# Performance work log

Hardware: AMD Instinct MI355X
Metric: run time of the kernel (lower is better)

The kernel has to match this reference:

```python
import jax, jax.numpy as jnp
import numpy as np

DIM = 768


def setup_inputs() -> dict:
    key = jax.random.key(0)
    k1, k2, k3, k4, k5 = jax.random.split(key, 5)
    lines = jax.random.normal(k1, (32, 512, DIM), dtype=jnp.float32)
    videos = jax.random.normal(k2, (32, 128, DIM), dtype=jnp.float32)
    video_mask = jax.random.randint(k3, (32, 128), 0, 2, dtype=jnp.int32)
    # nn.Linear(dim, dim, bias=False) weights, applied as x @ W.T
    w_q = jax.random.normal(k4, (DIM, DIM), dtype=jnp.float32) * (DIM ** -0.5)
    w_k = jax.random.normal(k5, (DIM, DIM), dtype=jnp.float32) * (DIM ** -0.5)
    return {"lines": lines, "videos": videos, "video_mask": video_mask, "w_q": w_q, "w_k": w_k}


def reference(lines, videos, video_mask, w_q, w_k):
    scale = DIM ** -0.5
    q = jnp.einsum('bld,ed->ble', lines, w_q)   # (B, L, D)
    k = jnp.einsum('bvd,ed->bve', videos, w_k)  # (B, V, D)
    scores = jnp.einsum('bld,bvd->blv', q, k) * scale
    pad = (video_mask == 0)[:, None, :]          # (B, 1, V)
    scores = jnp.where(pad, jnp.float32(-1e9), scores)
    weights = jax.nn.softmax(scores, axis=-1)    # (B, L, V)
    return jnp.einsum('blv,bvd->bld', weights, videos)
```

## Files before the change

### kernel.cpp

```cpp
#include <hip/hip_runtime.h>

#define DIM 768
#define NB  32
#define LQ  512
#define NV  128

typedef unsigned short u16;
typedef unsigned int   u32;
typedef __bf16 bf16x8 __attribute__((ext_vector_type(8)));
typedef float  f32x4  __attribute__((ext_vector_type(4)));
typedef u16    u16x8  __attribute__((ext_vector_type(8)));
typedef u16    u16x4  __attribute__((ext_vector_type(4)));

typedef __attribute__((address_space(1))) const void gvoid;
typedef __attribute__((address_space(3))) void       svoid;

__device__ __forceinline__ u16 f2bf(float f) {
    u32 u = __float_as_uint(f);
    return (u16)((u + 0x7FFFu + ((u >> 16) & 1u)) >> 16);
}

__device__ __forceinline__ bf16x8 ld_frag(const u16* p) {
    return __builtin_bit_cast(bf16x8, *(const u16x8*)p);
}

__device__ __forceinline__ void gld16(const void* g, void* l) {
    __builtin_amdgcn_global_load_lds((gvoid*)g, (svoid*)l, 16, 0, 0);
}

#define W2_BLK 36
#define NL_BLK 6144

__global__ __launch_bounds__(256) void prep_kernel(const float* __restrict__ lines,
                                                   const float* __restrict__ w_q,
                                                   const float* __restrict__ w_k,
                                                   const float* __restrict__ videos,
                                                   u16* __restrict__ lbf,
                                                   u16* __restrict__ w2b,
                                                   u16* __restrict__ vt2,
                                                   u16* __restrict__ vbf) {
    __shared__ union {
        u16 T[64][136];
        struct { u16 q[128][72]; u16 k[128][72]; } w2s;
    } uL;
    const int bx = blockIdx.x;
    const int t  = threadIdx.x;

    if (bx < W2_BLK) {
        const int m0 = (bx / 6) * 128;
        const int n0 = (bx % 6) * 128;
        const int w    = t >> 6;
        const int lane = t & 63;
        const int quad = lane >> 4;
        const int ln   = lane & 15;
        const int wr   = (w >> 1) * 64;
        const int wc   = (w & 1) * 64;
        f32x4 acc[4][4] = {};
        for (int ks = 0; ks < 12; ++ks) {
            __syncthreads();
            const int e0 = ks * 64;
#pragma unroll
            for (int p = 0; p < 8; ++p) {
                int f  = t + p * 256;
                int r  = f >> 5;
                int c4 = f & 31;
                float4 xq = *(const float4*)(w_q + (size_t)(e0 + r) * DIM + m0 + c4 * 4);
                float4 xk = *(const float4*)(w_k + (size_t)(e0 + r) * DIM + n0 + c4 * 4);
                uL.w2s.q[c4 * 4 + 0][r] = f2bf(xq.x);
                uL.w2s.q[c4 * 4 + 1][r] = f2bf(xq.y);
                uL.w2s.q[c4 * 4 + 2][r] = f2bf(xq.z);
                uL.w2s.q[c4 * 4 + 3][r] = f2bf(xq.w);
                uL.w2s.k[c4 * 4 + 0][r] = f2bf(xk.x);
                uL.w2s.k[c4 * 4 + 1][r] = f2bf(xk.y);
                uL.w2s.k[c4 * 4 + 2][r] = f2bf(xk.z);
                uL.w2s.k[c4 * 4 + 3][r] = f2bf(xk.w);
            }
            __syncthreads();
#pragma unroll
            for (int kk = 0; kk < 2; ++kk) {
                bf16x8 af[4], bfr[4];
#pragma unroll
                for (int i = 0; i < 4; ++i) af[i]  = ld_frag(&uL.w2s.q[wr + i * 16 + ln][kk * 32 + quad * 8]);
#pragma unroll
                for (int j = 0; j < 4; ++j) bfr[j] = ld_frag(&uL.w2s.k[wc + j * 16 + ln][kk * 32 + quad * 8]);
#pragma unroll
                for (int i = 0; i < 4; ++i)
#pragma unroll
                    for (int j = 0; j < 4; ++j)
                        acc[i][j] = __builtin_amdgcn_mfma_f32_16x16x32_bf16(af[i], bfr[j], acc[i][j], 0, 0, 0);
            }
        }
#pragma unroll
        for (int i = 0; i < 4; ++i)
#pragma unroll
            for (int j = 0; j < 4; ++j)
#pragma unroll
                for (int r = 0; r < 4; ++r)
                    w2b[(size_t)(m0 + wr + i * 16 + quad * 4 + r) * DIM + n0 + wc + j * 16 + ln] =
                        f2bf(acc[i][j][r]);
        return;
    }

    if (bx < W2_BLK + NL_BLK) {
        size_t i = (size_t)(bx - W2_BLK) * 256 + t;
        float4 a = ((const float4*)lines)[i * 2];
        float4 b = ((const float4*)lines)[i * 2 + 1];
        u16x8 o = { f2bf(a.x), f2bf(a.y), f2bf(a.z), f2bf(a.w),
                    f2bf(b.x), f2bf(b.y), f2bf(b.z), f2bf(b.w) };
        ((u16x8*)lbf)[i] = o;
        return;
    }

    const int v  = bx - (W2_BLK + NL_BLK);
    const int b  = v / 12;
    const int d0 = (v % 12) * 64;
    const float* src = videos + (size_t)b * NV * DIM;
#pragma unroll
    for (int p = 0; p < 8; ++p) {
        int f  = t + p * 256;
        int vv = f >> 4;
        int c4 = f & 15;
        float4 x = *(const float4*)(src + (size_t)vv * DIM + d0 + c4 * 4);
        u16x4 o = { f2bf(x.x), f2bf(x.y), f2bf(x.z), f2bf(x.w) };
        uL.T[c4 * 4 + 0][vv] = o[0];
        uL.T[c4 * 4 + 1][vv] = o[1];
        uL.T[c4 * 4 + 2][vv] = o[2];
        uL.T[c4 * 4 + 3][vv] = o[3];
        *(u16x4*)(vbf + ((size_t)b * NV + vv) * DIM + d0 + c4 * 4) = o;
    }
    __syncthreads();
#pragma unroll
    for (int p = 0; p < 4; ++p) {
        int f  = t + p * 256;
        int dl = f >> 4;
        int v8 = f & 15;
        int d  = d0 + dl;
        int it = d >> 7, wv = (d >> 4) & 7, lnn = d & 15;
        int ks = v8 >> 2, qd = v8 & 3;
        int lane = qd * 16 + lnn;
        size_t off = ((((size_t)b * 6 + it) * 8 + wv) * 4 + ks) * 512 + lane * 8;
        *(u16x8*)(vt2 + off) = *(const u16x8*)&uL.T[dl][v8 * 8];
    }
}

__global__ __launch_bounds__(512) void g_kernel(const u16* __restrict__ A,
                                                const u16* __restrict__ W,
                                                u16* __restrict__ C) {
    __shared__ u16 sA[128][64];
    __shared__ u16 sB[128][64];
    const int t    = threadIdx.x;
    const int w    = t >> 6;
    const int lane = t & 63;
    const int quad = lane >> 4;
    const int ln   = lane & 15;

    int m0, n0;
    {
        int i = blockIdx.x;
        int xcd = i & 7, s = i >> 3;
        m0 = ((s / 6) * 8 + xcd) * 128;
        n0 = (s % 6) * 128;
    }

    const int wr = (w >> 2) * 64;
    const int wc = (w & 3) * 32;
    const int srow   = lane >> 3;
    const int schunk = (lane & 7) ^ srow;

    f32x4 acc[4][2] = {};
#pragma unroll
    for (int ks = 0; ks < 12; ++ks) {
        __syncthreads();
#pragma unroll
        for (int p = 0; p < 2; ++p) {
            int rb = w * 16 + p * 8;
            gld16(A + (size_t)(m0 + rb + srow) * DIM + ks * 64 + schunk * 8, &sA[rb][0]);
            gld16(W + (size_t)(n0 + rb + srow) * DIM + ks * 64 + schunk * 8, &sB[rb][0]);
        }
        __syncthreads();
#pragma unroll
        for (int kk = 0; kk < 2; ++kk) {
            bf16x8 af[4], bfr[2];
#pragma unroll
            for (int i = 0; i < 4; ++i)
                af[i]  = ld_frag(&sA[wr + i * 16 + ln][((kk * 4 + quad) ^ (ln & 7)) * 8]);
#pragma unroll
            for (int j = 0; j < 2; ++j)
                bfr[j] = ld_frag(&sB[wc + j * 16 + ln][((kk * 4 + quad) ^ (ln & 7)) * 8]);
#pragma unroll
            for (int i = 0; i < 4; ++i)
#pragma unroll
                for (int j = 0; j < 2; ++j)
                    acc[i][j] = __builtin_amdgcn_mfma_f32_16x16x32_bf16(af[i], bfr[j], acc[i][j], 0, 0, 0);
        }
    }
#pragma unroll
    for (int i = 0; i < 4; ++i)
#pragma unroll
        for (int j = 0; j < 2; ++j)
#pragma unroll
            for (int r = 0; r < 4; ++r)
                C[(size_t)(m0 + wr + i * 16 + quad * 4 + r) * DIM + n0 + wc + j * 16 + ln] =
                    f2bf(acc[i][j][r]);
}

__global__ __launch_bounds__(512) void attn_kernel(const u16* __restrict__ Q,
                                                   const u16* __restrict__ K,
                                                   const u16* __restrict__ Vt2,
                                                   const int* __restrict__ mask,
                                                   float* __restrict__ out) {
    int b, l0;
    {
        int i = blockIdx.x;
        int xcd = i & 7, s = i >> 3;
        b  = (s >> 3) * 8 + xcd;
        l0 = (s & 7) * 64;
    }
    const int t    = threadIdx.x;
    const int w    = t >> 6;
    const int lane = t & 63;
    const int quad = lane >> 4;
    const int ln   = lane & 15;

    __shared__ union {
        struct { u16 q[64][64]; u16 k[128][64]; } st;
        float s[64][132];
    } uA;
    __shared__ union {
        struct { u16 q[64][64]; u16 k[128][64]; } st;
        u16 p[64][136];
    } uB;
    __shared__ float sBias[128];

    const u16* Qb = Q + ((size_t)b * LQ + l0) * DIM;
    const u16* Kb = K + (size_t)b * NV * DIM;
    if (t < NV) sBias[t] = mask[b * NV + t] ? 0.0f : -1e9f;

    const int srow   = lane >> 3;
    const int schunk = (lane & 7) ^ srow;

    auto stage = [&](int ks, int sel) {
        u16 (*q)[64] = sel ? uB.st.q : uA.st.q;
        u16 (*k)[64] = sel ? uB.st.k : uA.st.k;
        gld16(Qb + (size_t)(w * 8 + srow) * DIM + ks * 64 + schunk * 8, &q[w * 8][0]);
        gld16(Kb + (size_t)(w * 16 + srow) * DIM + ks * 64 + schunk * 8, &k[w * 16][0]);
        gld16(Kb + (size_t)(w * 16 + 8 + srow) * DIM + ks * 64 + schunk * 8, &k[w * 16 + 8][0]);
    };

    f32x4 accS[4] = {};
    stage(0, 0);
#pragma unroll
    for (int ks = 0; ks < 12; ++ks) {
        __syncthreads();
        if (ks < 11) stage(ks + 1, (ks + 1) & 1);
        u16 (*q)[64] = (ks & 1) ? uB.st.q : uA.st.q;
        u16 (*k)[64] = (ks & 1) ? uB.st.k : uA.st.k;
#pragma unroll
        for (int kk = 0; kk < 2; ++kk) {
            bf16x8 bfr = ld_frag(&k[w * 16 + ln][((kk * 4 + quad) ^ (ln & 7)) * 8]);
#pragma unroll
            for (int i = 0; i < 4; ++i) {
                bf16x8 af = ld_frag(&q[i * 16 + ln][((kk * 4 + quad) ^ (ln & 7)) * 8]);
                accS[i] = __builtin_amdgcn_mfma_f32_16x16x32_bf16(af, bfr, accS[i], 0, 0, 0);
            }
        }
    }
    __syncthreads();
    const float scale = 0.03608439182435161f;
#pragma unroll
    for (int i = 0; i < 4; ++i)
#pragma unroll
        for (int r = 0; r < 4; ++r)
            uA.s[i * 16 + quad * 4 + r][w * 16 + ln] = accS[i][r] * scale;
    __syncthreads();

    {
        const int row = t >> 3, seg = t & 7;
        float vals[16];
        float mx = -3.0e38f;
#pragma unroll
        for (int c = 0; c < 4; ++c) {
            float4 x  = *(const float4*)&uA.s[row][seg * 16 + c * 4];
            float4 bz = *(const float4*)&sBias[seg * 16 + c * 4];
            float a0 = x.x + bz.x, a1 = x.y + bz.y, a2 = x.z + bz.z, a3 = x.w + bz.w;
            vals[c * 4 + 0] = a0; vals[c * 4 + 1] = a1;
            vals[c * 4 + 2] = a2; vals[c * 4 + 3] = a3;
            mx = fmaxf(mx, fmaxf(fmaxf(a0, a1), fmaxf(a2, a3)));
        }
        mx = fmaxf(mx, __shfl_xor(mx, 1));
        mx = fmaxf(mx, __shfl_xor(mx, 2));
        mx = fmaxf(mx, __shfl_xor(mx, 4));
        float sum = 0.0f;
#pragma unroll
        for (int c = 0; c < 16; ++c) { float e = __expf(vals[c] - mx); vals[c] = e; sum += e; }
        sum += __shfl_xor(sum, 1);
        sum += __shfl_xor(sum, 2);
        sum += __shfl_xor(sum, 4);
        const float inv = 1.0f / sum;
        __syncthreads();
#pragma unroll
        for (int h = 0; h < 2; ++h) {
            u16x8 pk;
#pragma unroll
            for (int e = 0; e < 8; ++e) pk[e] = f2bf(vals[h * 8 + e] * inv);
            *(u16x8*)&uB.p[row][seg * 16 + h * 8] = pk;
        }
    }
    __syncthreads();

    bf16x8 paf[4][4];
#pragma unroll
    for (int i = 0; i < 4; ++i)
#pragma unroll
        for (int ks = 0; ks < 4; ++ks)
            paf[i][ks] = ld_frag(&uB.p[i * 16 + ln][ks * 32 + quad * 8]);

    const u16* V2 = Vt2 + (size_t)b * 6 * 8 * 4 * 512;
    float*     Ob = out + ((size_t)b * LQ + l0) * DIM;
    for (int it = 0; it < 6; ++it) {
        f32x4 accO[4] = {};
#pragma unroll
        for (int ks = 0; ks < 4; ++ks) {
            bf16x8 bv = ld_frag(V2 + (((size_t)(it * 8 + w)) * 4 + ks) * 512 + lane * 8);
#pragma unroll
            for (int i = 0; i < 4; ++i)
                accO[i] = __builtin_amdgcn_mfma_f32_16x16x32_bf16(paf[i][ks], bv, accO[i], 0, 0, 0);
        }
#pragma unroll
        for (int i = 0; i < 4; ++i)
#pragma unroll
            for (int r = 0; r < 4; ++r)
                Ob[(size_t)(i * 16 + quad * 4 + r) * DIM + it * 128 + w * 16 + ln] = accO[i][r];
    }
}

extern "C" void kernel_launch(void* const* d_in, const int* in_sizes, int n_in,
                              void* d_out, int out_size, void* d_ws, size_t ws_size,
                              hipStream_t stream) {
    const float* lines  = (const float*)d_in[0];
    const float* videos = (const float*)d_in[1];
    const int*   mask   = (const int*)d_in[2];
    const float* w_q    = (const float*)d_in[3];
    const float* w_k    = (const float*)d_in[4];
    float*       out    = (float*)d_out;

    u16* gw  = (u16*)d_ws;
    u16* vt2 = gw  + (size_t)NB * NV * DIM;
    u16* lbf = vt2 + (size_t)NB * DIM * NV;
    u16* vbf = lbf + (size_t)NB * LQ * DIM;
    u16* w2b = vbf + (size_t)NB * NV * DIM;

    prep_kernel<<<W2_BLK + NL_BLK + 384, 256, 0, stream>>>(
        lines, w_q, w_k, videos, lbf, w2b, vt2, vbf);
    g_kernel   <<<192, 512, 0, stream>>>(vbf, w2b, gw);
    attn_kernel<<<256, 512, 0, stream>>>(lbf, gw, vt2, mask, out);
}
```

Measured before the change: 192.6 us.

## Split W_q^T W_k product over K with atomic fp32 accumulation and swizzled LDS

The W2 = Wq^T·Wk tile blocks are split four ways along the reduction dimension, so 144 blocks run instead of 36, and the partial sums are combined with float atomicAdd into an fp32 buffer that is zeroed by a memset first. The LDS tiles in that GEMM get an XOR swizzle to cut bank conflicts on transposed stores and fragment loads. g_kernel now reads the fp32 W2 and converts it to bf16 into a padded, swizzled LDS tile, in place of the async global-to-LDS copy of bf16 data. This is meant to shorten the tail of the prep kernel, where a few long-running W2 blocks finish late. In exchange it adds a memset launch, atomic traffic, and heavier per-block loads and conversion in g_kernel.

```diff
diff --git a/kernel.cpp b/kernel.cpp
--- a/kernel.cpp
+++ b/kernel.cpp
@@ -28,7 +28,8 @@
     __builtin_amdgcn_global_load_lds((gvoid*)g, (svoid*)l, 16, 0, 0);
 }
 
-#define W2_BLK 36
+#define W2S    4
+#define W2_BLK (36 * W2S)
 #define NL_BLK 6144
 
 __global__ __launch_bounds__(256) void prep_kernel(const float* __restrict__ lines,
@@ -36,7 +37,7 @@
                                                    const float* __restrict__ w_k,
                                                    const float* __restrict__ videos,
                                                    u16* __restrict__ lbf,
-                                                   u16* __restrict__ w2b,
+                                                   float* __restrict__ w2f,
                                                    u16* __restrict__ vt2,
                                                    u16* __restrict__ vbf) {
     __shared__ union {
@@ -47,8 +48,9 @@
     const int t  = threadIdx.x;
 
     if (bx < W2_BLK) {
-        const int m0 = (bx / 6) * 128;
-        const int n0 = (bx % 6) * 128;
+        const int tile = bx / W2S, kc = bx % W2S;
+        const int m0 = (tile / 6) * 128;
+        const int n0 = (tile % 6) * 128;
         const int w    = t >> 6;
         const int lane = t & 63;
         const int quad = lane >> 4;
@@ -56,7 +58,7 @@
         const int wr   = (w >> 1) * 64;
         const int wc   = (w & 1) * 64;
         f32x4 acc[4][4] = {};
-        for (int ks = 0; ks < 12; ++ks) {
+        for (int ks = kc * 3; ks < kc * 3 + 3; ++ks) {
             __syncthreads();
             const int e0 = ks * 64;
 #pragma unroll
@@ -66,23 +68,30 @@
                 int c4 = f & 31;
                 float4 xq = *(const float4*)(w_q + (size_t)(e0 + r) * DIM + m0 + c4 * 4);
                 float4 xk = *(const float4*)(w_k + (size_t)(e0 + r) * DIM + n0 + c4 * 4);
-                uL.w2s.q[c4 * 4 + 0][r] = f2bf(xq.x);
-                uL.w2s.q[c4 * 4 + 1][r] = f2bf(xq.y);
-                uL.w2s.q[c4 * 4 + 2][r] = f2bf(xq.z);
-                uL.w2s.q[c4 * 4 + 3][r] = f2bf(xq.w);
-                uL.w2s.k[c4 * 4 + 0][r] = f2bf(xk.x);
-                uL.w2s.k[c4 * 4 + 1][r] = f2bf(xk.y);
-                uL.w2s.k[c4 * 4 + 2][r] = f2bf(xk.z);
-                uL.w2s.k[c4 * 4 + 3][r] = f2bf(xk.w);
+                int swz = ((r >> 3) ^ ((c4 >> 1) & 7)) * 8 + (r & 7);
+                uL.w2s.q[c4 * 4 + 0][swz] = f2bf(xq.x);
+                uL.w2s.q[c4 * 4 + 1][swz] = f2bf(xq.y);
+                uL.w2s.q[c4 * 4 + 2][swz] = f2bf(xq.z);
+                uL.w2s.q[c4 * 4 + 3][swz] = f2bf(xq.w);
+                uL.w2s.k[c4 * 4 + 0][swz] = f2bf(xk.x);
+                uL.w2s.k[c4 * 4 + 1][swz] = f2bf(xk.y);
+                uL.w2s.k[c4 * 4 + 2][swz] = f2bf(xk.z);
+                uL.w2s.k[c4 * 4 + 3][swz] = f2bf(xk.w);
             }
             __syncthreads();
 #pragma unroll
             for (int kk = 0; kk < 2; ++kk) {
                 bf16x8 af[4], bfr[4];
 #pragma unroll
-                for (int i = 0; i < 4; ++i) af[i]  = ld_frag(&uL.w2s.q[wr + i * 16 + ln][kk * 32 + quad * 8]);
-#pragma unroll
-                for (int j = 0; j < 4; ++j) bfr[j] = ld_frag(&uL.w2s.k[wc + j * 16 + ln][kk * 32 + quad * 8]);
+                for (int i = 0; i < 4; ++i) {
+                    int row = wr + i * 16 + ln;
+                    af[i]  = ld_frag(&uL.w2s.q[row][((kk * 4 + quad) ^ ((row >> 3) & 7)) * 8]);
+                }
+#pragma unroll
+                for (int j = 0; j < 4; ++j) {
+                    int row = wc + j * 16 + ln;
+                    bfr[j] = ld_frag(&uL.w2s.k[row][((kk * 4 + quad) ^ ((row >> 3) & 7)) * 8]);
+                }
 #pragma unroll
                 for (int i = 0; i < 4; ++i)
 #pragma unroll
@@ -96,8 +105,8 @@
             for (int j = 0; j < 4; ++j)
 #pragma unroll
                 for (int r = 0; r < 4; ++r)
-                    w2b[(size_t)(m0 + wr + i * 16 + quad * 4 + r) * DIM + n0 + wc + j * 16 + ln] =
-                        f2bf(acc[i][j][r]);
+                    atomicAdd(&w2f[(size_t)(m0 + wr + i * 16 + quad * 4 + r) * DIM +
+                                   n0 + wc + j * 16 + ln], acc[i][j][r]);
         return;
     }
 
@@ -144,10 +153,10 @@
 }
 
 __global__ __launch_bounds__(512) void g_kernel(const u16* __restrict__ A,
-                                                const u16* __restrict__ W,
+                                                const float* __restrict__ Wf,
                                                 u16* __restrict__ C) {
     __shared__ u16 sA[128][64];
-    __shared__ u16 sB[128][64];
+    __shared__ u16 sB[128][72];
     const int t    = threadIdx.x;
     const int w    = t >> 6;
     const int lane = t & 63;
@@ -175,7 +184,15 @@
         for (int p = 0; p < 2; ++p) {
             int rb = w * 16 + p * 8;
             gld16(A + (size_t)(m0 + rb + srow) * DIM + ks * 64 + schunk * 8, &sA[rb][0]);
-            gld16(W + (size_t)(n0 + rb + srow) * DIM + ks * 64 + schunk * 8, &sB[rb][0]);
+        }
+#pragma unroll
+        for (int p = 0; p < 4; ++p) {
+            int idx = t + p * 512;
+            int row = idx >> 4, c4 = idx & 15;
+            float4 x = *(const float4*)(Wf + (size_t)(n0 + row) * DIM + ks * 64 + c4 * 4);
+            u16x4 o = { f2bf(x.x), f2bf(x.y), f2bf(x.z), f2bf(x.w) };
+            int swz = ((c4 >> 1) ^ (row & 7)) * 8 + (c4 & 1) * 4;
+            *(u16x4*)&sB[row][swz] = o;
         }
         __syncthreads();
 #pragma unroll
@@ -344,14 +361,15 @@
     const float* w_k    = (const float*)d_in[4];
     float*       out    = (float*)d_out;
 
-    u16* gw  = (u16*)d_ws;
-    u16* vt2 = gw  + (size_t)NB * NV * DIM;
-    u16* lbf = vt2 + (size_t)NB * DIM * NV;
-    u16* vbf = lbf + (size_t)NB * LQ * DIM;
-    u16* w2b = vbf + (size_t)NB * NV * DIM;
-
+    u16*   gw  = (u16*)d_ws;
+    u16*   vt2 = gw  + (size_t)NB * NV * DIM;
+    u16*   lbf = vt2 + (size_t)NB * DIM * NV;
+    u16*   vbf = lbf + (size_t)NB * LQ * DIM;
+    float* w2f = (float*)(vbf + (size_t)NB * NV * DIM);
+
+    hipMemsetAsync(w2f, 0, (size_t)DIM * DIM * sizeof(float), stream);
     prep_kernel<<<W2_BLK + NL_BLK + 384, 256, 0, stream>>>(
-        lines, w_q, w_k, videos, lbf, w2b, vt2, vbf);
-    g_kernel   <<<192, 512, 0, stream>>>(vbf, w2b, gw);
+        lines, w_q, w_k, videos, lbf, w2f, vt2, vbf);
+    g_kernel   <<<192, 512, 0, stream>>>(vbf, w2f, gw);
     attn_kernel<<<256, 512, 0, stream>>>(lbf, gw, vt2, mask, out);
 }
```

After: 163.6 us. 1.18x faster.
